# Performance work log

Measured on AMD Instinct MI355X. Metric: run time of the kernel, lower is better.

The kernel has to match this reference:

```python
import jax, jax.numpy as jnp
import numpy as np

B, N, D_IN, D_OUT, L, T = 8, 512, 1024, 1024, 16, 4096


def setup_inputs() -> dict:
    key = jax.random.key(0)
    k1, k2, k3 = jax.random.split(key, 3)
    pooled_vectors = jax.random.normal(k1, (B, N, D_IN), dtype=jnp.float32)
    # stacked nn.Linear weights, each (out, in), bias=False
    W = jax.random.normal(k2, (L, D_OUT, D_IN), dtype=jnp.float32) * 0.02
    pooling_indices = jnp.sort(jax.random.randint(k3, (N,), 0, T, dtype=jnp.int64))
    return {
        "pooled_vectors": pooled_vectors,
        "W": W,
        "pooling_indices": pooling_indices,
        "target_length": T,
    }


def reference(pooled_vectors, W, pooling_indices, target_length):
    # pooled_vectors: (B, N, D_in); W: (L, D_out, D_in); pooling_indices: (N,) sorted
    Bn, Nn, _ = pooled_vectors.shape
    Ln = W.shape[0]
    t = jnp.arange(target_length)
    # segment i covers [start_i, idx_i + 1); searchsorted finds the covering segment
    seg = jnp.searchsorted(pooling_indices, t, side="left")  # (T,)
    valid = seg < Nn  # positions past the last pooling index stay zero
    segc = jnp.clip(seg, 0, Nn - 1)
    start = jnp.where(segc > 0, pooling_indices[segc - 1] + 1, 0)
    lidx = jnp.minimum(t - start, Ln - 1)  # position-specific linear index, capped
    # apply all L position linears to every pooled vector: (B, N, L, D_out)
    trans = jnp.einsum("bnd,lod->bnlo", pooled_vectors, W)
    out = trans[:, segc, lidx]  # gather per output position -> (B, T, D_out)
    return jnp.where(valid[None, :, None], out, jnp.zeros((), out.dtype))
```

## Files before the change

kernel.cpp:

```cpp
#include <hip/hip_runtime.h>
#include <stdint.h>

#define B_    8
#define N_    512
#define DIN   1024
#define DOUT  1024
#define L_    16
#define T_    4096

#define BM 256
#define BN 256
#define BK 64
#define NB (DOUT / BN)
#define NKT (DIN / BK)
#define NIT (NKT / 2)
#define MT_MAX 160
#define ZROW ((long)B_ * N_)

typedef __attribute__((ext_vector_type(8))) short short8;
typedef __attribute__((ext_vector_type(4))) float f32x4;

#define POOLED_ELEMS ((long)B_ * N_ * DIN + DIN)
#define WS_W_OFF     ((size_t)POOLED_ELEMS * 2)
#define WS_META_OFF  (WS_W_OFF + (size_t)L_ * DOUT * DIN * 2)

__device__ __forceinline__ unsigned short f2bf(float f) {
  unsigned u = __float_as_uint(f);
  u += 0x7FFFu + ((u >> 16) & 1u);
  return (unsigned short)(u >> 16);
}

__device__ __forceinline__ void gload_lds16(const void* g, void* l) {
  __builtin_amdgcn_global_load_lds(
      (const __attribute__((address_space(1))) void*)g,
      (__attribute__((address_space(3))) void*)l, 16, 0, 0);
}

__device__ __forceinline__ void bar() {
  asm volatile("" ::: "memory");
  __builtin_amdgcn_s_barrier();
  asm volatile("" ::: "memory");
}

__global__ void k_convert(const float* __restrict__ pooled,
                          const float* __restrict__ W,
                          unsigned short* __restrict__ wsP,
                          unsigned short* __restrict__ wsW) {
  const long np4 = (long)B_ * N_ * DIN / 4;
  const long nw4 = (long)L_ * DOUT * DIN / 4;
  const long nz4 = DIN / 4;
  long i = (long)blockIdx.x * blockDim.x + threadIdx.x;
  const long stride = (long)gridDim.x * blockDim.x;
  for (; i < np4 + nw4 + nz4; i += stride) {
    if (i < np4) {
      float4 v = ((const float4*)pooled)[i];
      ushort4 o = { f2bf(v.x), f2bf(v.y), f2bf(v.z), f2bf(v.w) };
      ((ushort4*)wsP)[i] = o;
    } else if (i < np4 + nw4) {
      float4 v = ((const float4*)W)[i - np4];
      ushort4 o = { f2bf(v.x), f2bf(v.y), f2bf(v.z), f2bf(v.w) };
      ((ushort4*)wsW)[i - np4] = o;
    } else {
      ushort4 z = {0, 0, 0, 0};
      ((ushort4*)wsP)[i - nw4] = z;
    }
  }
}

__global__ void k_prep(const int* __restrict__ pidx,
                       unsigned* __restrict__ tlist,
                       int* __restrict__ goff, int* __restrict__ grows,
                       unsigned* __restrict__ table, int* __restrict__ ntiles) {
  __shared__ int sp[N_];
  __shared__ unsigned smap[T_];
  __shared__ int cnt[L_], pos[L_];
  const int tid = threadIdx.x;
  for (int i = tid; i < N_; i += 256) sp[i] = pidx[i];
  if (tid < L_) cnt[tid] = 0;
  __syncthreads();
  for (int t = tid; t < T_; t += 256) {
    int lo = 0, hi = N_;
    while (lo < hi) { int mid = (lo + hi) >> 1; if (sp[mid] < t) lo = mid + 1; else hi = mid; }
    int n, l;
    if (lo < N_) {
      int start = lo ? sp[lo - 1] + 1 : 0;
      int li = t - start;
      l = li > (L_ - 1) ? (L_ - 1) : li;
      n = lo;
    } else { n = 0xFFFF; l = L_ - 1; }
    smap[t] = (unsigned)n | ((unsigned)l << 16);
    atomicAdd(&cnt[l], 1);
  }
  __syncthreads();
  if (tid == 0) {
    int off = 0;
    for (int l = 0; l < L_; ++l) {
      pos[l] = off; goff[l] = off; grows[l] = cnt[l] * B_;
      off += cnt[l];
    }
  }
  __syncthreads();
  for (int t = tid; t < T_; t += 256) {
    unsigned m = smap[t];
    int l = m >> 16;
    int p = atomicAdd(&pos[l], 1);
    tlist[p] = (unsigned)t | ((m & 0xFFFFu) << 16);
  }
  __syncthreads();
  if (tid == 0) {
    int tt = 0;
    for (int l = 0; l < L_; ++l) {
      int rows = cnt[l] * B_;
      for (int r0 = 0; r0 < rows; r0 += BM) table[tt++] = (unsigned)l | ((unsigned)r0 << 4);
    }
    *ntiles = tt;
  }
}

__global__ __launch_bounds__(512, 2)
void k_gemm(const unsigned short* __restrict__ wsP,
            const unsigned short* __restrict__ wsW,
            const unsigned* __restrict__ tlist,
            const int* __restrict__ goff,
            const int* __restrict__ grows,
            const unsigned* __restrict__ table,
            const int* __restrict__ ntiles,
            float* __restrict__ out) {
  const int bid = blockIdx.x;
  const int mt = bid >> 2;
  const int nt = bid & 3;
  if (mt >= *ntiles) return;

  const unsigned te = table[mt];
  const int l    = te & 15;
  const int row0 = (int)(te >> 4);
  const int toff = goff[l];
  const int rows = grows[l];

  __shared__ __align__(16) unsigned short As[2][BM * BK];
  __shared__ __align__(16) unsigned short Bs[2][BN * BK];

  const int tid  = threadIdx.x;
  const int lane = tid & 63;
  const int w    = tid >> 6;
  const int wm   = w >> 2;
  const int wn   = w & 3;

  const int srow = tid >> 3;
  const int sxor = ((tid & 7) ^ (srow & 7)) * 16;
  const char* aptr[4];
  const char* bptr[4];
#pragma unroll
  for (int h = 0; h < 2; ++h)
#pragma unroll
    for (int r = 0; r < 2; ++r) {
      int rt = h * 128 + r * 64 + srow;
      int rg = row0 + rt;
      long rowElem;
      if (rg < rows) {
        unsigned e = tlist[toff + (rg >> 3)];
        unsigned n = e >> 16;
        int b = rg & 7;
        rowElem = (n == 0xFFFFu) ? ZROW * (long)DIN
                                 : ((long)(b * N_ + (int)n)) * DIN;
      } else rowElem = ZROW * (long)DIN;
      aptr[h * 2 + r] = (const char*)(wsP + rowElem) + sxor;
      bptr[h * 2 + r] = (const char*)(wsW + ((long)l * DOUT + nt * BN + rt) * DIN) + sxor;
    }

#define STG_A(h, kt, bb) do { \
  gload_lds16(aptr[(h)*2+0] + (kt)*128, (char*)As[bb] + (((h)*128 + w*8)*128)); \
  gload_lds16(aptr[(h)*2+1] + (kt)*128, (char*)As[bb] + (((h)*128 + 64 + w*8)*128)); } while (0)
#define STG_B(h, kt, bb) do { \
  gload_lds16(bptr[(h)*2+0] + (kt)*128, (char*)Bs[bb] + (((h)*128 + w*8)*128)); \
  gload_lds16(bptr[(h)*2+1] + (kt)*128, (char*)Bs[bb] + (((h)*128 + 64 + w*8)*128)); } while (0)

  const int aoff = (wm * 128 + (lane & 15)) * 128;
  const int boff = (wn * 64  + (lane & 15)) * 128;
  const int ax0  = (((lane >> 4)    ) ^ (lane & 7)) * 16;
  const int ax1  = (((lane >> 4) + 4) ^ (lane & 7)) * 16;

#define DS_AF(bb, mo) do { _Pragma("unroll") \
  for (int m_ = 0; m_ < 4; ++m_) { \
    af[m_][0] = *(const short8*)((const char*)As[bb] + aoff + ((mo)+m_)*2048 + ax0); \
    af[m_][1] = *(const short8*)((const char*)As[bb] + aoff + ((mo)+m_)*2048 + ax1); } } while (0)
#define DS_BF(bb, no) do { _Pragma("unroll") \
  for (int n_ = 0; n_ < 2; ++n_) { \
    bf[(no)+n_][0] = *(const short8*)((const char*)Bs[bb] + boff + ((no)+n_)*2048 + ax0); \
    bf[(no)+n_][1] = *(const short8*)((const char*)Bs[bb] + boff + ((no)+n_)*2048 + ax1); } } while (0)
#define QUAD(mo, no) do { _Pragma("unroll") \
  for (int n_ = 0; n_ < 2; ++n_) { _Pragma("unroll") \
    for (int m_ = 0; m_ < 4; ++m_) { \
      acc[(mo)+m_][(no)+n_] = __builtin_amdgcn_mfma_f32_16x16x32_bf16(af[m_][0], bf[(no)+n_][0], acc[(mo)+m_][(no)+n_], 0, 0, 0); \
      acc[(mo)+m_][(no)+n_] = __builtin_amdgcn_mfma_f32_16x16x32_bf16(af[m_][1], bf[(no)+n_][1], acc[(mo)+m_][(no)+n_], 0, 0, 0); } } } while (0)
#define LGKM0 asm volatile("s_waitcnt lgkmcnt(0)" ::: "memory")
#define P1 __builtin_amdgcn_s_setprio(1)
#define P0 __builtin_amdgcn_s_setprio(0)

  f32x4 acc[8][4];
#pragma unroll
  for (int m = 0; m < 8; ++m)
#pragma unroll
    for (int n = 0; n < 4; ++n)
      acc[m][n] = (f32x4){0.f, 0.f, 0.f, 0.f};

  short8 af[4][2], bf[4][2];

  STG_A(0, 0, 0); STG_A(1, 0, 0); STG_B(0, 0, 0); STG_B(1, 0, 0);
  STG_A(0, 1, 1);
  asm volatile("s_waitcnt vmcnt(2)" ::: "memory");
  bar();

  for (int j = 0; j < NIT; ++j) {
    const int t1 = 2 * j + 1, t2 = 2 * j + 2, t3 = 2 * j + 3;

    DS_AF(0, 0); DS_BF(0, 0);
    STG_A(1, t1, 1);
    bar(); LGKM0; P1; QUAD(0, 0); P0; bar();

    DS_BF(0, 2);
    STG_B(0, t1, 1);
    bar(); LGKM0; P1; QUAD(0, 2); P0; bar();

    DS_AF(0, 4);
    STG_B(1, t1, 1);
    bar(); LGKM0; P1; QUAD(4, 0); P0; bar();

    if (t2 < NKT) STG_A(0, t2, 0);
    bar(); P1; QUAD(4, 2); P0;
    if (j < NIT - 1) asm volatile("s_waitcnt vmcnt(2)" ::: "memory");
    else             asm volatile("s_waitcnt vmcnt(0)" ::: "memory");
    bar();

    DS_AF(1, 0); DS_BF(1, 0);
    if (t2 < NKT) STG_A(1, t2, 0);
    bar(); LGKM0; P1; QUAD(0, 0); P0; bar();

    DS_BF(1, 2);
    if (t2 < NKT) STG_B(0, t2, 0);
    bar(); LGKM0; P1; QUAD(0, 2); P0; bar();

    DS_AF(1, 4);
    if (t2 < NKT) STG_B(1, t2, 0);
    bar(); LGKM0; P1; QUAD(4, 0); P0; bar();

    if (t3 < NKT) STG_A(0, t3, 1);
    bar(); P1; QUAD(4, 2); P0;
    if (j < NIT - 1) asm volatile("s_waitcnt vmcnt(2)" ::: "memory");
    bar();
  }

#pragma unroll
  for (int m = 0; m < 8; ++m) {
#pragma unroll
    for (int jj = 0; jj < 4; ++jj) {
      int rt = wm * 128 + m * 16 + (lane >> 4) * 4 + jj;
      int rg = row0 + rt;
      if (rg >= rows) continue;
      unsigned e = tlist[toff + (rg >> 3)];
      int b = rg & 7;
      int tt = (int)(e & 0xFFFFu);
      float* orow = out + ((long)b * T_ + tt) * DOUT + nt * BN + wn * 64 + (lane & 15);
#pragma unroll
      for (int n = 0; n < 4; ++n)
        orow[n * 16] = acc[m][n][jj];
    }
  }
#undef STG_A
#undef STG_B
#undef DS_AF
#undef DS_BF
#undef QUAD
#undef LGKM0
#undef P1
#undef P0
}

extern "C" void kernel_launch(void* const* d_in, const int* in_sizes, int n_in,
                              void* d_out, int out_size, void* d_ws, size_t ws_size,
                              hipStream_t stream) {
  const float* pooled = (const float*)d_in[0];
  const float* W      = (const float*)d_in[1];
  const int*   pidx   = (const int*)d_in[2];
  float* out = (float*)d_out;

  char* ws = (char*)d_ws;
  unsigned short* wsP = (unsigned short*)(ws);
  unsigned short* wsW = (unsigned short*)(ws + WS_W_OFF);
  int* meta  = (int*)(ws + WS_META_OFF);
  unsigned* tlist = (unsigned*)meta;
  int* goff  = meta + T_;
  int* grows = meta + T_ + 16;
  unsigned* table = (unsigned*)(meta + T_ + 32);
  int* ntiles = meta + T_ + 32 + MT_MAX;

  k_prep<<<1, 256, 0, stream>>>(pidx, tlist, goff, grows, table, ntiles);
  k_convert<<<2048, 256, 0, stream>>>(pooled, W, wsP, wsW);
  k_gemm<<<MT_MAX * NB, 512, 0, stream>>>(wsP, wsW, tlist, goff, grows, table,
                                          ntiles, out);
}
```

Baseline: 149.7 us.

## Shrink GEMM tile to 256x128x32 with three-stage LDS pipeline

Halves the N tile and the K step, doubling the number of N-tiles per M-tile. The two-stage, quad-split schedule becomes a simpler three-buffer pipeline that issues one phase per K step, and the launch bound now requests more resident blocks. The aim is more blocks in flight and a simpler, deeper prefetch that better hides load latency. In exchange, operand reuse per tile drops, the A rows are fetched more times overall, and there are more barriers per FLOP.

Measured after the change: 141.8 us. 5.3% less time.

```diff
diff --git a/kernel.cpp b/kernel.cpp
--- a/kernel.cpp
+++ b/kernel.cpp
@@ -9,11 +9,10 @@
 #define T_    4096
 
 #define BM 256
-#define BN 256
-#define BK 64
+#define BN 128
+#define BK 32
 #define NB (DOUT / BN)
 #define NKT (DIN / BK)
-#define NIT (NKT / 2)
 #define MT_MAX 160
 #define ZROW ((long)B_ * N_)
 
@@ -117,7 +116,7 @@
   }
 }
 
-__global__ __launch_bounds__(512, 2)
+__global__ __launch_bounds__(512, 4)
 void k_gemm(const unsigned short* __restrict__ wsP,
             const unsigned short* __restrict__ wsW,
             const unsigned* __restrict__ tlist,
@@ -127,8 +126,8 @@
             const int* __restrict__ ntiles,
             float* __restrict__ out) {
   const int bid = blockIdx.x;
-  const int mt = bid >> 2;
-  const int nt = bid & 3;
+  const int mt = bid >> 3;
+  const int nt = bid & 7;
   if (mt >= *ntiles) return;
 
   const unsigned te = table[mt];
@@ -137,124 +136,91 @@
   const int toff = goff[l];
   const int rows = grows[l];
 
-  __shared__ __align__(16) unsigned short As[2][BM * BK];
-  __shared__ __align__(16) unsigned short Bs[2][BN * BK];
+  __shared__ __align__(16) unsigned short As[3][BM * BK];
+  __shared__ __align__(16) unsigned short Bs[3][BN * BK];
 
   const int tid  = threadIdx.x;
   const int lane = tid & 63;
   const int w    = tid >> 6;
-  const int wm   = w >> 2;
-  const int wn   = w & 3;
-
-  const int srow = tid >> 3;
-  const int sxor = ((tid & 7) ^ (srow & 7)) * 16;
-  const char* aptr[4];
-  const char* bptr[4];
-#pragma unroll
-  for (int h = 0; h < 2; ++h)
+  const int wm   = w >> 1;
+  const int wn   = w & 1;
+
+  const int srow = tid >> 2;
+  const int sx4  = ((tid & 3) ^ (srow & 3)) * 16;
+  const char* aptr0;
+  const char* aptr1;
+  {
+    long re[2];
 #pragma unroll
     for (int r = 0; r < 2; ++r) {
-      int rt = h * 128 + r * 64 + srow;
-      int rg = row0 + rt;
-      long rowElem;
+      int rg = row0 + r * 128 + srow;
       if (rg < rows) {
         unsigned e = tlist[toff + (rg >> 3)];
         unsigned n = e >> 16;
         int b = rg & 7;
-        rowElem = (n == 0xFFFFu) ? ZROW * (long)DIN
-                                 : ((long)(b * N_ + (int)n)) * DIN;
-      } else rowElem = ZROW * (long)DIN;
-      aptr[h * 2 + r] = (const char*)(wsP + rowElem) + sxor;
-      bptr[h * 2 + r] = (const char*)(wsW + ((long)l * DOUT + nt * BN + rt) * DIN) + sxor;
-    }
-
-#define STG_A(h, kt, bb) do { \
-  gload_lds16(aptr[(h)*2+0] + (kt)*128, (char*)As[bb] + (((h)*128 + w*8)*128)); \
-  gload_lds16(aptr[(h)*2+1] + (kt)*128, (char*)As[bb] + (((h)*128 + 64 + w*8)*128)); } while (0)
-#define STG_B(h, kt, bb) do { \
-  gload_lds16(bptr[(h)*2+0] + (kt)*128, (char*)Bs[bb] + (((h)*128 + w*8)*128)); \
-  gload_lds16(bptr[(h)*2+1] + (kt)*128, (char*)Bs[bb] + (((h)*128 + 64 + w*8)*128)); } while (0)
-
-  const int aoff = (wm * 128 + (lane & 15)) * 128;
-  const int boff = (wn * 64  + (lane & 15)) * 128;
-  const int ax0  = (((lane >> 4)    ) ^ (lane & 7)) * 16;
-  const int ax1  = (((lane >> 4) + 4) ^ (lane & 7)) * 16;
-
-#define DS_AF(bb, mo) do { _Pragma("unroll") \
-  for (int m_ = 0; m_ < 4; ++m_) { \
-    af[m_][0] = *(const short8*)((const char*)As[bb] + aoff + ((mo)+m_)*2048 + ax0); \
-    af[m_][1] = *(const short8*)((const char*)As[bb] + aoff + ((mo)+m_)*2048 + ax1); } } while (0)
-#define DS_BF(bb, no) do { _Pragma("unroll") \
-  for (int n_ = 0; n_ < 2; ++n_) { \
-    bf[(no)+n_][0] = *(const short8*)((const char*)Bs[bb] + boff + ((no)+n_)*2048 + ax0); \
-    bf[(no)+n_][1] = *(const short8*)((const char*)Bs[bb] + boff + ((no)+n_)*2048 + ax1); } } while (0)
-#define QUAD(mo, no) do { _Pragma("unroll") \
-  for (int n_ = 0; n_ < 2; ++n_) { _Pragma("unroll") \
-    for (int m_ = 0; m_ < 4; ++m_) { \
-      acc[(mo)+m_][(no)+n_] = __builtin_amdgcn_mfma_f32_16x16x32_bf16(af[m_][0], bf[(no)+n_][0], acc[(mo)+m_][(no)+n_], 0, 0, 0); \
-      acc[(mo)+m_][(no)+n_] = __builtin_amdgcn_mfma_f32_16x16x32_bf16(af[m_][1], bf[(no)+n_][1], acc[(mo)+m_][(no)+n_], 0, 0, 0); } } } while (0)
-#define LGKM0 asm volatile("s_waitcnt lgkmcnt(0)" ::: "memory")
-#define P1 __builtin_amdgcn_s_setprio(1)
-#define P0 __builtin_amdgcn_s_setprio(0)
-
-  f32x4 acc[8][4];
-#pragma unroll
-  for (int m = 0; m < 8; ++m)
+        re[r] = (n == 0xFFFFu) ? ZROW * (long)DIN
+                               : ((long)(b * N_ + (int)n)) * DIN;
+      } else re[r] = ZROW * (long)DIN;
+    }
+    aptr0 = (const char*)(wsP + re[0]) + sx4;
+    aptr1 = (const char*)(wsP + re[1]) + sx4;
+  }
+  const char* bptr = (const char*)(wsW + ((long)l * DOUT + nt * BN + srow) * DIN) + sx4;
+
+#define STG(t_, sb) do { \
+  gload_lds16(aptr0 + (t_) * 64, (char*)As[sb] + w * 1024); \
+  gload_lds16(aptr1 + (t_) * 64, (char*)As[sb] + 8192 + w * 1024); \
+  gload_lds16(bptr  + (t_) * 64, (char*)Bs[sb] + w * 1024); } while (0)
+
+  const int arow = wm * 64 + (lane & 15);
+  const int brow = wn * 64 + (lane & 15);
+  const int axr  = ((lane >> 4) ^ (lane & 3)) * 16;
+
+  f32x4 acc[4][4];
+#pragma unroll
+  for (int m = 0; m < 4; ++m)
 #pragma unroll
     for (int n = 0; n < 4; ++n)
       acc[m][n] = (f32x4){0.f, 0.f, 0.f, 0.f};
 
-  short8 af[4][2], bf[4][2];
-
-  STG_A(0, 0, 0); STG_A(1, 0, 0); STG_B(0, 0, 0); STG_B(1, 0, 0);
-  STG_A(0, 1, 1);
-  asm volatile("s_waitcnt vmcnt(2)" ::: "memory");
+  short8 af[4], bf[4];
+
+#define PHASE(t_, bb, sb) do { \
+  const int t2_ = (t_) + 2; \
+  if (t2_ < NKT) STG(t2_, sb); \
+  _Pragma("unroll") for (int m_ = 0; m_ < 4; ++m_) \
+    af[m_] = *(const short8*)((const char*)As[bb] + (arow + m_ * 16) * 64 + axr); \
+  _Pragma("unroll") for (int n_ = 0; n_ < 4; ++n_) \
+    bf[n_] = *(const short8*)((const char*)Bs[bb] + (brow + n_ * 16) * 64 + axr); \
+  bar(); \
+  asm volatile("s_waitcnt lgkmcnt(0)" ::: "memory"); \
+  __builtin_amdgcn_s_setprio(1); \
+  _Pragma("unroll") for (int n_ = 0; n_ < 4; ++n_) \
+    _Pragma("unroll") for (int m_ = 0; m_ < 4; ++m_) \
+      acc[m_][n_] = __builtin_amdgcn_mfma_f32_16x16x32_bf16(af[m_], bf[n_], acc[m_][n_], 0, 0, 0); \
+  __builtin_amdgcn_s_setprio(0); \
+  if (t2_ < NKT) asm volatile("s_waitcnt vmcnt(3)" ::: "memory"); \
+  else           asm volatile("s_waitcnt vmcnt(0)" ::: "memory"); \
+  bar(); \
+} while (0)
+
+  STG(0, 0);
+  STG(1, 1);
+  asm volatile("s_waitcnt vmcnt(3)" ::: "memory");
   bar();
 
-  for (int j = 0; j < NIT; ++j) {
-    const int t1 = 2 * j + 1, t2 = 2 * j + 2, t3 = 2 * j + 3;
-
-    DS_AF(0, 0); DS_BF(0, 0);
-    STG_A(1, t1, 1);
-    bar(); LGKM0; P1; QUAD(0, 0); P0; bar();
-
-    DS_BF(0, 2);
-    STG_B(0, t1, 1);
-    bar(); LGKM0; P1; QUAD(0, 2); P0; bar();
-
-    DS_AF(0, 4);
-    STG_B(1, t1, 1);
-    bar(); LGKM0; P1; QUAD(4, 0); P0; bar();
-
-    if (t2 < NKT) STG_A(0, t2, 0);
-    bar(); P1; QUAD(4, 2); P0;
-    if (j < NIT - 1) asm volatile("s_waitcnt vmcnt(2)" ::: "memory");
-    else             asm volatile("s_waitcnt vmcnt(0)" ::: "memory");
-    bar();
-
-    DS_AF(1, 0); DS_BF(1, 0);
-    if (t2 < NKT) STG_A(1, t2, 0);
-    bar(); LGKM0; P1; QUAD(0, 0); P0; bar();
-
-    DS_BF(1, 2);
-    if (t2 < NKT) STG_B(0, t2, 0);
-    bar(); LGKM0; P1; QUAD(0, 2); P0; bar();
-
-    DS_AF(1, 4);
-    if (t2 < NKT) STG_B(1, t2, 0);
-    bar(); LGKM0; P1; QUAD(4, 0); P0; bar();
-
-    if (t3 < NKT) STG_A(0, t3, 1);
-    bar(); P1; QUAD(4, 2); P0;
-    if (j < NIT - 1) asm volatile("s_waitcnt vmcnt(2)" ::: "memory");
-    bar();
-  }
-
-#pragma unroll
-  for (int m = 0; m < 8; ++m) {
+  for (int j = 0; j < 11; ++j) {
+    const int t0 = 3 * j;
+    if (t0     < NKT) PHASE(t0,     0, 2);
+    if (t0 + 1 < NKT) PHASE(t0 + 1, 1, 0);
+    if (t0 + 2 < NKT) PHASE(t0 + 2, 2, 1);
+  }
+
+#pragma unroll
+  for (int m = 0; m < 4; ++m) {
 #pragma unroll
     for (int jj = 0; jj < 4; ++jj) {
-      int rt = wm * 128 + m * 16 + (lane >> 4) * 4 + jj;
+      int rt = wm * 64 + m * 16 + (lane >> 4) * 4 + jj;
       int rg = row0 + rt;
       if (rg >= rows) continue;
       unsigned e = tlist[toff + (rg >> 3)];
@@ -266,14 +232,8 @@
         orow[n * 16] = acc[m][n][jj];
     }
   }
-#undef STG_A
-#undef STG_B
-#undef DS_AF
-#undef DS_BF
-#undef QUAD
-#undef LGKM0
-#undef P1
-#undef P0
+#undef STG
+#undef PHASE
 }
 
 extern "C" void kernel_launch(void* const* d_in, const int* in_sizes, int n_in,
```

## Restructure GEMM main loop into k-half MFMA phases with B-first prefetch

Applied to the files above, without the earlier changes.

Reorganizes the inner loop of the grouped GEMM. Each k-tile is now processed in four phases, one per k-half and M-half, each issuing a full 4x4 block of MFMAs instead of 2x4 quads. Global-to-LDS prefetch is reordered so the next tile's B is staged before A, with waits changed to vmcnt(4). Launch bounds drop from 2 to 1 blocks per CU, which frees registers at the cost of occupancy, and MT_MAX is lowered to 144. The aim is fewer LDS reloads of B fragments and better overlap of loads with MFMA work.

Result: faster. 146.7 us (-2.0%).

```diff
diff --git a/kernel.cpp b/kernel.cpp
--- a/kernel.cpp
+++ b/kernel.cpp
@@ -14,7 +14,7 @@
 #define NB (DOUT / BN)
 #define NKT (DIN / BK)
 #define NIT (NKT / 2)
-#define MT_MAX 160
+#define MT_MAX 144
 #define ZROW ((long)B_ * N_)
 
 typedef __attribute__((ext_vector_type(8))) short short8;
@@ -117,7 +117,7 @@
   }
 }
 
-__global__ __launch_bounds__(512, 2)
+__global__ __launch_bounds__(512, 1)
 void k_gemm(const unsigned short* __restrict__ wsP,
             const unsigned short* __restrict__ wsW,
             const unsigned* __restrict__ tlist,
@@ -180,22 +180,21 @@
   const int ax0  = (((lane >> 4)    ) ^ (lane & 7)) * 16;
   const int ax1  = (((lane >> 4) + 4) ^ (lane & 7)) * 16;
 
-#define DS_AF(bb, mo) do { _Pragma("unroll") \
-  for (int m_ = 0; m_ < 4; ++m_) { \
-    af[m_][0] = *(const short8*)((const char*)As[bb] + aoff + ((mo)+m_)*2048 + ax0); \
-    af[m_][1] = *(const short8*)((const char*)As[bb] + aoff + ((mo)+m_)*2048 + ax1); } } while (0)
-#define DS_BF(bb, no) do { _Pragma("unroll") \
-  for (int n_ = 0; n_ < 2; ++n_) { \
-    bf[(no)+n_][0] = *(const short8*)((const char*)Bs[bb] + boff + ((no)+n_)*2048 + ax0); \
-    bf[(no)+n_][1] = *(const short8*)((const char*)Bs[bb] + boff + ((no)+n_)*2048 + ax1); } } while (0)
-#define QUAD(mo, no) do { _Pragma("unroll") \
-  for (int n_ = 0; n_ < 2; ++n_) { _Pragma("unroll") \
-    for (int m_ = 0; m_ < 4; ++m_) { \
-      acc[(mo)+m_][(no)+n_] = __builtin_amdgcn_mfma_f32_16x16x32_bf16(af[m_][0], bf[(no)+n_][0], acc[(mo)+m_][(no)+n_], 0, 0, 0); \
-      acc[(mo)+m_][(no)+n_] = __builtin_amdgcn_mfma_f32_16x16x32_bf16(af[m_][1], bf[(no)+n_][1], acc[(mo)+m_][(no)+n_], 0, 0, 0); } } } while (0)
+#define AF4(bb, mb, kh, AX) do { _Pragma("unroll") \
+  for (int m_ = 0; m_ < 4; ++m_) \
+    af[m_][kh] = *(const short8*)((const char*)As[bb] + aoff + ((mb)+m_)*2048 + (AX)); } while (0)
+#define BF4(bb, kh, AX) do { _Pragma("unroll") \
+  for (int n_ = 0; n_ < 4; ++n_) \
+    bf[n_][kh] = *(const short8*)((const char*)Bs[bb] + boff + n_*2048 + (AX)); } while (0)
+#define MM(mb, kh) do { _Pragma("unroll") \
+  for (int n_ = 0; n_ < 4; ++n_) { _Pragma("unroll") \
+    for (int m_ = 0; m_ < 4; ++m_) \
+      acc[(mb)+m_][n_] = __builtin_amdgcn_mfma_f32_16x16x32_bf16(af[m_][kh], bf[n_][kh], acc[(mb)+m_][n_], 0, 0, 0); } } while (0)
 #define LGKM0 asm volatile("s_waitcnt lgkmcnt(0)" ::: "memory")
 #define P1 __builtin_amdgcn_s_setprio(1)
 #define P0 __builtin_amdgcn_s_setprio(0)
+#define VMC4 asm volatile("s_waitcnt vmcnt(4)" ::: "memory")
+#define VMC0 asm volatile("s_waitcnt vmcnt(0)" ::: "memory")
 
   f32x4 acc[8][4];
 #pragma unroll
@@ -207,46 +206,48 @@
   short8 af[4][2], bf[4][2];
 
   STG_A(0, 0, 0); STG_A(1, 0, 0); STG_B(0, 0, 0); STG_B(1, 0, 0);
-  STG_A(0, 1, 1);
-  asm volatile("s_waitcnt vmcnt(2)" ::: "memory");
+  STG_B(0, 1, 1); STG_B(1, 1, 1);
+  VMC4;
   bar();
 
   for (int j = 0; j < NIT; ++j) {
     const int t1 = 2 * j + 1, t2 = 2 * j + 2, t3 = 2 * j + 3;
-
-    DS_AF(0, 0); DS_BF(0, 0);
+    const bool last = (j == NIT - 1);
+
+    AF4(0, 0, 0, ax0); BF4(0, 0, ax0);
+    STG_A(0, t1, 1);
+    bar(); LGKM0; P1; MM(0, 0); P0; bar();
+
+    AF4(0, 0, 1, ax1); BF4(0, 1, ax1);
     STG_A(1, t1, 1);
-    bar(); LGKM0; P1; QUAD(0, 0); P0; bar();
-
-    DS_BF(0, 2);
-    STG_B(0, t1, 1);
-    bar(); LGKM0; P1; QUAD(0, 2); P0; bar();
-
-    DS_AF(0, 4);
-    STG_B(1, t1, 1);
-    bar(); LGKM0; P1; QUAD(4, 0); P0; bar();
-
+    bar(); LGKM0; P1; MM(0, 1); P0; bar();
+
+    AF4(0, 4, 0, ax0);
+    if (t2 < NKT) STG_B(0, t2, 0);
+    bar(); LGKM0; P1; MM(4, 0); P0; bar();
+
+    AF4(0, 4, 1, ax1);
+    if (t2 < NKT) STG_B(1, t2, 0);
+    bar(); LGKM0; P1; MM(4, 1); P0;
+    if (last) VMC0; else VMC4;
+    bar();
+
+    AF4(1, 0, 0, ax0); BF4(1, 0, ax0);
     if (t2 < NKT) STG_A(0, t2, 0);
-    bar(); P1; QUAD(4, 2); P0;
-    if (j < NIT - 1) asm volatile("s_waitcnt vmcnt(2)" ::: "memory");
-    else             asm volatile("s_waitcnt vmcnt(0)" ::: "memory");
-    bar();
-
-    DS_AF(1, 0); DS_BF(1, 0);
+    bar(); LGKM0; P1; MM(0, 0); P0; bar();
+
+    AF4(1, 0, 1, ax1); BF4(1, 1, ax1);
     if (t2 < NKT) STG_A(1, t2, 0);
-    bar(); LGKM0; P1; QUAD(0, 0); P0; bar();
-
-    DS_BF(1, 2);
-    if (t2 < NKT) STG_B(0, t2, 0);
-    bar(); LGKM0; P1; QUAD(0, 2); P0; bar();
-
-    DS_AF(1, 4);
-    if (t2 < NKT) STG_B(1, t2, 0);
-    bar(); LGKM0; P1; QUAD(4, 0); P0; bar();
-
-    if (t3 < NKT) STG_A(0, t3, 1);
-    bar(); P1; QUAD(4, 2); P0;
-    if (j < NIT - 1) asm volatile("s_waitcnt vmcnt(2)" ::: "memory");
+    bar(); LGKM0; P1; MM(0, 1); P0; bar();
+
+    AF4(1, 4, 0, ax0);
+    if (t3 < NKT) STG_B(0, t3, 1);
+    bar(); LGKM0; P1; MM(4, 0); P0; bar();
+
+    AF4(1, 4, 1, ax1);
+    if (t3 < NKT) STG_B(1, t3, 1);
+    bar(); LGKM0; P1; MM(4, 1); P0;
+    if (last) VMC0; else VMC4;
     bar();
   }
 
@@ -268,12 +269,14 @@
   }
 #undef STG_A
 #undef STG_B
-#undef DS_AF
-#undef DS_BF
-#undef QUAD
+#undef AF4
+#undef BF4
+#undef MM
 #undef LGKM0
 #undef P1
 #undef P0
+#undef VMC4
+#undef VMC0
 }
 
 extern "C" void kernel_launch(void* const* d_in, const int* in_sizes, int n_in,
```
